# Kernel optimization log

Measured on AMD Instinct MI355X. Metric: run time of the kernel, lower is better.

The kernel has to match this reference:

```python
import jax, jax.numpy as jnp
import numpy as np

BEAM = 3
MAX_LENGTH = 32
START = 1


def setup_inputs() -> dict:
    key = jax.random.key(0)
    ks = jax.random.split(key, 10)
    B, S, H, E, V = 32, 64, 512, 256, 32000
    sE = 1.0 / np.sqrt(E)
    sH = 1.0 / np.sqrt(H)
    return {
        "encoder_outputs": jax.random.normal(ks[0], (B, S, H), jnp.float32),
        "encoder_hidden": jax.random.normal(ks[1], (B, H), jnp.float32),
        "emb": jax.random.normal(ks[2], (V, E), jnp.float32) * 0.02,
        "W_ih": jax.random.uniform(ks[3], (3 * H, E), jnp.float32, -sE, sE),
        "W_hh": jax.random.uniform(ks[4], (3 * H, H), jnp.float32, -sH, sH),
        "b_ih": jax.random.uniform(ks[5], (3 * H,), jnp.float32, -sH, sH),
        "b_hh": jax.random.uniform(ks[6], (3 * H,), jnp.float32, -sH, sH),
        "W_out": jax.random.uniform(ks[7], (V, H), jnp.float32, -sH, sH),
        "b_out": jax.random.uniform(ks[8], (V,), jnp.float32, -sH, sH),
    }


def _gru_cell(x, h, W_ih, W_hh, b_ih, b_hh):
    # PyTorch GRU cell math. x: (N,E), h: (N,H)
    gi = x @ W_ih.T + b_ih          # (N, 3H)
    gh = h @ W_hh.T + b_hh          # (N, 3H)
    i_r, i_z, i_n = jnp.split(gi, 3, axis=-1)
    h_r, h_z, h_n = jnp.split(gh, 3, axis=-1)
    r = jax.nn.sigmoid(i_r + h_r)
    z = jax.nn.sigmoid(i_z + h_z)
    n = jnp.tanh(i_n + r * h_n)
    return (1.0 - z) * n + z * h


def reference(encoder_outputs, encoder_hidden, emb, W_ih, W_hh, b_ih, b_hh, W_out, b_out):
    B = encoder_outputs.shape[0]
    K = BEAM
    V, H = W_out.shape
    BK = B * K

    # expand encoder hidden for beams: each batch row repeated K times
    h0 = jnp.repeat(encoder_hidden, K, axis=0)                 # (BK, H)
    tok0 = jnp.full((BK,), START, jnp.int32)
    seqs0 = jnp.full((BK, MAX_LENGTH + 1), START, jnp.int32)   # col 0 = start token
    scores0 = jnp.zeros((BK,), jnp.float32)
    brow = jnp.arange(B)[:, None] * K                          # (B,1)

    def step(carry, t):
        tok, h, seqs, scores = carry
        x = jax.nn.relu(emb[tok])                              # (BK, E) gather + relu
        h_new = _gru_cell(x, h, W_ih, W_hh, b_ih, b_hh)        # (BK, H)
        logits = h_new @ W_out.T + b_out                       # (BK, V)
        logp = jax.nn.log_softmax(logits, axis=-1)
        next_scores, next_tokens = jax.lax.top_k(logp, K)      # (BK, K)
        total = scores.reshape(B, K, 1) + next_scores.reshape(B, K, K)
        top_scores, top_idx = jax.lax.top_k(total.reshape(B, K * K), K)  # (B, K)
        beam_idx = top_idx // K
        tok_idx = top_idx % K
        old = (brow + beam_idx).reshape(-1)                    # (BK,) source beam rows
        new_tok = next_tokens[old, tok_idx.reshape(-1)].astype(jnp.int32)
        h2 = h_new[old]
        seqs2 = jax.lax.dynamic_update_slice(seqs[old], new_tok[:, None], (0, t + 1))
        return (new_tok, h2, seqs2, top_scores.reshape(-1)), None

    (tok, h, seqs, scores), _ = jax.lax.scan(
        step, (tok0, h0, seqs0, scores0), jnp.arange(MAX_LENGTH))

    # beam 0 is best (top_k is sorted descending)
    best_seqs = seqs.reshape(B, K, MAX_LENGTH + 1)[:, 0]       # (B, L+1)
    decoded = jax.nn.one_hot(best_seqs, V, dtype=jnp.float32)  # (B, L+1, V)
    return decoded, h.reshape(B, K, H), scores.reshape(B, K)
```

## Files before the change

kernel.cpp:

```cpp
#include <hip/hip_runtime.h>
#include <float.h>
#include <math.h>


#define BB 32
#define HH 512
#define EE 256
#define VV 32000
#define TSTEPS 32
#define NCH 500
#define PSTR 512
#define DEC_ELEMS (BB * (TSTEPS + 1) * VV)
#define H_ELEMS (BB * 3 * HH)
#define SMEM_FLOATS 18432
#define HB (BB * HH)
#define SB (BB * PSTR)

__device__ __forceinline__ void st_agent(float* p, float v) {
  __hip_atomic_store(p, v, __ATOMIC_RELAXED, __HIP_MEMORY_SCOPE_AGENT);
}
__device__ __forceinline__ void st_agent_i(int* p, int v) {
  __hip_atomic_store(p, v, __ATOMIC_RELAXED, __HIP_MEMORY_SCOPE_AGENT);
}

__global__ __launch_bounds__(256) void k_transpose_out(
    const float* __restrict__ W, float* __restrict__ Wt) {
  __shared__ float t[32][33];
  const int vb = blockIdx.x * 32;
  const int kb = blockIdx.y * 32;
  const int c = threadIdx.x & 31, rq = threadIdx.x >> 5;
#pragma unroll
  for (int i = 0; i < 4; ++i) {
    int r = rq + i * 8;
    t[r][c] = W[(size_t)(vb + r) * HH + kb + c];
  }
  __syncthreads();
#pragma unroll
  for (int i = 0; i < 4; ++i) {
    int r = rq + i * 8;
    Wt[(size_t)(kb + r) * VV + vb + c] = t[c][r];
  }
}

__global__ __launch_bounds__(256) void k_init(
    const float* __restrict__ enc_h, float* __restrict__ h0,
    float* __restrict__ scores, int* __restrict__ tok_seq,
    unsigned* __restrict__ bar) {
  int idx = blockIdx.x * 256 + threadIdx.x;
  if (idx < BB * HH) h0[idx] = enc_h[idx];
  if (idx < BB) { scores[idx] = 0.0f; tok_seq[idx] = 1; }
  if (idx == 0) { bar[0] = 0u; bar[32] = 0u; }
}

__device__ __forceinline__ void gbar(unsigned* bar, unsigned nblk) {
  __syncthreads();
  if (threadIdx.x == 0) {
    asm volatile("s_waitcnt vmcnt(0)" ::: "memory");
    unsigned g = __hip_atomic_load(&bar[32], __ATOMIC_RELAXED,
                                   __HIP_MEMORY_SCOPE_AGENT);
    asm volatile("s_waitcnt vmcnt(0)" ::: "memory");
    unsigned a = __hip_atomic_fetch_add(&bar[0], 1u, __ATOMIC_RELAXED,
                                        __HIP_MEMORY_SCOPE_AGENT);
    if (a == nblk - 1u) {
      __hip_atomic_store(&bar[0], 0u, __ATOMIC_RELAXED,
                         __HIP_MEMORY_SCOPE_AGENT);
      asm volatile("s_waitcnt vmcnt(0)" ::: "memory");
      __hip_atomic_fetch_add(&bar[32], 1u, __ATOMIC_RELAXED,
                             __HIP_MEMORY_SCOPE_AGENT);
    } else {
      while (__hip_atomic_load(&bar[32], __ATOMIC_RELAXED,
                               __HIP_MEMORY_SCOPE_AGENT) == g)
        __builtin_amdgcn_s_sleep(2);
    }
  }
  __syncthreads();
}

#define FMA4(accv, hscal, wv)              \
  accv.x = fmaf(hscal, wv.x, accv.x);      \
  accv.y = fmaf(hscal, wv.y, accv.y);      \
  accv.z = fmaf(hscal, wv.z, accv.z);      \
  accv.w = fmaf(hscal, wv.w, accv.w);

#define LOADG(W, g)                                                    \
  {                                                                    \
    const float* p_ = wp + (size_t)(g) * 8 * VV;                       \
    _Pragma("unroll") for (int j_ = 0; j_ < 8; ++j_)                   \
        W[j_] = *(const float4*)(p_ + (size_t)j_ * VV);                \
  }

#define COMPG(W, g)                                                    \
  {                                                                    \
    const int k0_ = (g) * 8;                                           \
    _Pragma("unroll") for (int jj_ = 0; jj_ < 2; ++jj_) {              \
      const float4 h0_ = *(const float4*)&hs[r0][k0_ + jj_ * 4];       \
      const float4 h1_ = *(const float4*)&hs[r0 + 1][k0_ + jj_ * 4];   \
      FMA4(acc0, h0_.x, W[jj_ * 4 + 0]);                               \
      FMA4(acc0, h0_.y, W[jj_ * 4 + 1]);                               \
      FMA4(acc0, h0_.z, W[jj_ * 4 + 2]);                               \
      FMA4(acc0, h0_.w, W[jj_ * 4 + 3]);                               \
      FMA4(acc1, h1_.x, W[jj_ * 4 + 0]);                               \
      FMA4(acc1, h1_.y, W[jj_ * 4 + 1]);                               \
      FMA4(acc1, h1_.z, W[jj_ * 4 + 2]);                               \
      FMA4(acc1, h1_.w, W[jj_ * 4 + 3]);                               \
    }                                                                  \
  }

__device__ __forceinline__ void gemv_body_glb(
    const int vb, const int tid, float* smem,
    const float* __restrict__ Wt, const float* __restrict__ hmat,
    const float* __restrict__ bout,
    float* __restrict__ pm, float* __restrict__ ps, int* __restrict__ pidx) {
  const int colq = tid & 15;
  const int rp = tid >> 4;
  const int r0 = rp * 2;
  const int col = vb * 64 + colq * 4;

  float (*hs)[516] = (float(*)[516])smem;
  {
    float4* hd = (float4*)smem;
    const float4* hp = (const float4*)hmat;
#pragma unroll
    for (int i = 0; i < 16; ++i) {
      const int idx = i * 256 + tid;
      const int r = idx >> 7, q = idx & 127;
      hd[r * 129 + q] = hp[idx];
    }
  }
  __syncthreads();

  const float* wp = Wt + col;
  float4 acc0 = {0.0f, 0.0f, 0.0f, 0.0f};
  float4 acc1 = {0.0f, 0.0f, 0.0f, 0.0f};

  float4 A[8], B[8], C[8];
  LOADG(A, 0);
  LOADG(B, 1);
#pragma unroll 1
  for (int g = 0; g < 63; g += 3) {
    LOADG(C, g + 2);
    COMPG(A, g);
    if (g + 3 < 64) LOADG(A, g + 3);
    COMPG(B, g + 1);
    if (g + 4 < 64) LOADG(B, g + 4);
    COMPG(C, g + 2);
  }
  COMPG(A, 63);

  {
    const float4 bo = *(const float4*)(bout + col);
    acc0.x += bo.x; acc0.y += bo.y; acc0.z += bo.z; acc0.w += bo.w;
    acc1.x += bo.x; acc1.y += bo.y; acc1.z += bo.z; acc1.w += bo.w;
  }

  const int lane = tid & 63;
  float m0 = acc0.x; int i0 = col;
  if (acc0.y > m0) { m0 = acc0.y; i0 = col + 1; }
  if (acc0.z > m0) { m0 = acc0.z; i0 = col + 2; }
  if (acc0.w > m0) { m0 = acc0.w; i0 = col + 3; }
  float m1 = acc1.x; int i1 = col;
  if (acc1.y > m1) { m1 = acc1.y; i1 = col + 1; }
  if (acc1.z > m1) { m1 = acc1.z; i1 = col + 2; }
  if (acc1.w > m1) { m1 = acc1.w; i1 = col + 3; }
#pragma unroll
  for (int off = 1; off < 16; off <<= 1) {
    const float om0 = __shfl_xor(m0, off);
    const int oi0 = __shfl_xor(i0, off);
    if (om0 > m0 || (om0 == m0 && oi0 < i0)) { m0 = om0; i0 = oi0; }
    const float om1 = __shfl_xor(m1, off);
    const int oi1 = __shfl_xor(i1, off);
    if (om1 > m1 || (om1 == m1 && oi1 < i1)) { m1 = om1; i1 = oi1; }
  }
  float s0 = __expf(acc0.x - m0) + __expf(acc0.y - m0) +
             __expf(acc0.z - m0) + __expf(acc0.w - m0);
  float s1 = __expf(acc1.x - m1) + __expf(acc1.y - m1) +
             __expf(acc1.z - m1) + __expf(acc1.w - m1);
#pragma unroll
  for (int off = 1; off < 16; off <<= 1) {
    s0 += __shfl_xor(s0, off);
    s1 += __shfl_xor(s1, off);
  }
  if ((lane & 15) == 0) {
    st_agent(&pm[r0 * PSTR + vb], m0);
    st_agent(&ps[r0 * PSTR + vb], s0);
    st_agent_i(&pidx[r0 * PSTR + vb], i0);
    st_agent(&pm[(r0 + 1) * PSTR + vb], m1);
    st_agent(&ps[(r0 + 1) * PSTR + vb], s1);
    st_agent_i(&pidx[(r0 + 1) * PSTR + vb], i1);
  }
}

__device__ __forceinline__ void gru_body(
    const int bid, const int tid, const int step, float* smem, int* toks,
    const float* __restrict__ emb,
    const float* __restrict__ W_ih,
    const float* __restrict__ W_hh,
    const float* __restrict__ b_ih, const float* __restrict__ b_hh,
    const float* __restrict__ hin, float* __restrict__ hout,
    const float* __restrict__ pmt, const float* __restrict__ pst,
    const int* __restrict__ pidxt,
    float* __restrict__ scores, int* __restrict__ tok_seq) {
  const int rg = bid >> 4;
  const int jt = bid & 15;
  const int r0 = rg * 4, j0 = jt * 32;
  const int lane = tid & 63, wv = tid >> 6;

  float (*xs)[EE] = (float(*)[EE])smem;
  float (*hsm)[HH] = (float(*)[HH])(smem + 4 * EE);
  float* gpart = smem + 4 * EE + 4 * HH;

  if (step == 0) {
    if (tid < 4) toks[tid] = 1;
  } else {
    const int row = r0 + wv;
    float mv[8], sv[8];
    int iv[8];
#pragma unroll
    for (int j = 0; j < 8; ++j) {
      const int ch = lane + 64 * j;
      const bool v = (ch < NCH);
      mv[j] = v ? pmt[row * PSTR + ch] : -FLT_MAX;
      sv[j] = v ? pst[row * PSTR + ch] : 0.0f;
      iv[j] = v ? pidxt[row * PSTR + ch] : 0x7fffffff;
    }
    float gm = mv[0];
    int gi = iv[0];
#pragma unroll
    for (int j = 1; j < 8; ++j)
      if (mv[j] > gm || (mv[j] == gm && iv[j] < gi)) { gm = mv[j]; gi = iv[j]; }
#pragma unroll
    for (int off = 1; off < 64; off <<= 1) {
      const float om = __shfl_xor(gm, off);
      const int oi = __shfl_xor(gi, off);
      if (om > gm || (om == gm && oi < gi)) { gm = om; gi = oi; }
    }
    float term = 0.0f;
#pragma unroll
    for (int j = 0; j < 8; ++j) term += sv[j] * __expf(mv[j] - gm);
#pragma unroll
    for (int off = 1; off < 64; off <<= 1) term += __shfl_xor(term, off);
    if (lane == 0) {
      toks[wv] = gi;
      if (jt == 0) {
        scores[row] -= logf(term);
        tok_seq[step * BB + row] = gi;
      }
    }
  }
  __syncthreads();
  if (step == TSTEPS) return;

  for (int i = tid; i < 4 * EE; i += 256) {
    const int r = i >> 8, c = i & (EE - 1);
    const float e = emb[(size_t)toks[r] * EE + c];
    xs[r][c] = e > 0.0f ? e : 0.0f;
  }
  for (int i = tid; i < 4 * HH; i += 256) {
    const int r = i >> 9, c = i & (HH - 1);
    hsm[r][c] = hin[(r0 + r) * HH + c];
  }
  __syncthreads();

  const int jh = tid & 31, kq = tid >> 5;
  const int j = j0 + jh;
  float ai[3][4], ah[3][4];
#pragma unroll
  for (int g = 0; g < 3; ++g)
#pragma unroll
    for (int r = 0; r < 4; ++r) { ai[g][r] = 0.0f; ah[g][r] = 0.0f; }

#pragma unroll 2
  for (int q = 0; q < 8; ++q) {
    const int k4 = kq * 32 + q * 4;
    float4 xr[4];
#pragma unroll
    for (int r = 0; r < 4; ++r) xr[r] = *(const float4*)&xs[r][k4];
#pragma unroll
    for (int g = 0; g < 3; ++g) {
      const float4 w = *(const float4*)&W_ih[(size_t)(g * HH + j) * EE + k4];
#pragma unroll
      for (int r = 0; r < 4; ++r) {
        ai[g][r] = fmaf(xr[r].x, w.x, ai[g][r]);
        ai[g][r] = fmaf(xr[r].y, w.y, ai[g][r]);
        ai[g][r] = fmaf(xr[r].z, w.z, ai[g][r]);
        ai[g][r] = fmaf(xr[r].w, w.w, ai[g][r]);
      }
    }
  }
#pragma unroll 2
  for (int q = 0; q < 16; ++q) {
    const int k4 = kq * 64 + q * 4;
    float4 hr[4];
#pragma unroll
    for (int r = 0; r < 4; ++r) hr[r] = *(const float4*)&hsm[r][k4];
#pragma unroll
    for (int g = 0; g < 3; ++g) {
      const float4 w = *(const float4*)&W_hh[(size_t)(g * HH + j) * HH + k4];
#pragma unroll
      for (int r = 0; r < 4; ++r) {
        ah[g][r] = fmaf(hr[r].x, w.x, ah[g][r]);
        ah[g][r] = fmaf(hr[r].y, w.y, ah[g][r]);
        ah[g][r] = fmaf(hr[r].z, w.z, ah[g][r]);
        ah[g][r] = fmaf(hr[r].w, w.w, ah[g][r]);
      }
    }
  }
  {
    const int base = kq * 34 + jh;
#pragma unroll
    for (int g = 0; g < 3; ++g)
#pragma unroll
      for (int r = 0; r < 4; ++r) {
        gpart[(g * 4 + r) * 272 + base] = ai[g][r];
        gpart[(12 + g * 4 + r) * 272 + base] = ah[g][r];
      }
  }
  __syncthreads();

  if (tid < 128) {
    const int r = tid >> 5, jh2 = tid & 31;
    const int j2 = j0 + jh2;
    float g6[6];
#pragma unroll
    for (int c = 0; c < 6; ++c) {
      const int cc = (c < 3) ? (c * 4 + r) : (12 + (c - 3) * 4 + r);
      float s = 0.0f;
#pragma unroll
      for (int q = 0; q < 8; ++q) s += gpart[cc * 272 + q * 34 + jh2];
      g6[c] = s;
    }
    const float ir = g6[0] + b_ih[j2];
    const float iz = g6[1] + b_ih[HH + j2];
    const float in_ = g6[2] + b_ih[2 * HH + j2];
    const float hr_ = g6[3] + b_hh[j2];
    const float hz = g6[4] + b_hh[HH + j2];
    const float hn = g6[5] + b_hh[2 * HH + j2];
    const float rr = 1.0f / (1.0f + expf(-(ir + hr_)));
    const float zz = 1.0f / (1.0f + expf(-(iz + hz)));
    const float nn = tanhf(in_ + rr * hn);
    st_agent(&hout[(r0 + r) * HH + j2], (1.0f - zz) * nn + zz * hsm[r][j2]);
  }
}

__global__ __launch_bounds__(256, 2) void k_persist(
    const float* __restrict__ Wt, const float* __restrict__ emb,
    const float* __restrict__ W_ih, const float* __restrict__ W_hh,
    const float* __restrict__ b_ih, const float* __restrict__ b_hh,
    const float* __restrict__ bout,
    float* hseq, float* pmT, float* psT, int* pidxT,
    float* scores, int* tok_seq, unsigned* bar) {
  __shared__ __align__(16) float smem[SMEM_FLOATS];
  __shared__ int toks[4];
  const int bid = blockIdx.x, tid = threadIdx.x;
  const int c2 = tid & 31, kq = tid >> 5;
  const int vb = bid;

  float2 wreg[64];
  if (vb < NCH) {
    const float* wp = Wt + (size_t)(kq * 64) * VV + vb * 64 + c2 * 2;
#pragma unroll
    for (int k = 0; k < 64; ++k)
      wreg[k] = *(const float2*)(wp + (size_t)k * VV);
  } else {
#pragma unroll
    for (int k = 0; k < 64; ++k) wreg[k] = make_float2(0.0f, 0.0f);
  }
  float2 bo = make_float2(0.0f, 0.0f);
  if (vb < NCH) bo = *(const float2*)(bout + vb * 64 + c2 * 2);

  float* hs = smem;
  float* part = smem + 16384;

  for (int t = 0; t <= TSTEPS; ++t) {
    const float* hin = hseq + (size_t)t * HB;
    float* hout = hseq + (size_t)(t + 1) * HB;
    const int tp = (t > 0) ? (t - 1) : 0;
    if (bid < 128)
      gru_body(bid, tid, t, smem, toks, emb, W_ih, W_hh, b_ih, b_hh,
               hin, hout, pmT + (size_t)tp * SB, psT + (size_t)tp * SB,
               pidxT + (size_t)tp * SB, scores, tok_seq);
    gbar(bar, 512u);
    if (t == TSTEPS) break;

    if (vb < NCH) {
      float* pm = pmT + (size_t)t * SB;
      float* ps = psT + (size_t)t * SB;
      int* pidx = pidxT + (size_t)t * SB;
      {
        float4* hd = (float4*)hs;
        const float4* hp = (const float4*)hout;
#pragma unroll
        for (int i = 0; i < 16; ++i) hd[i * 256 + tid] = hp[i * 256 + tid];
      }
      __syncthreads();

      const int w = tid >> 6;
      const int rr = tid >> 5;
      const int cp = tid & 31;
#pragma unroll 1
      for (int rc = 0; rc < 4; ++rc) {
        float acc0[8], acc1[8];
#pragma unroll
        for (int r = 0; r < 8; ++r) { acc0[r] = 0.0f; acc1[r] = 0.0f; }
#pragma unroll
        for (int r = 0; r < 8; ++r) {
          const float* hrow = hs + (rc * 8 + r) * 512 + kq * 64;
#pragma unroll
          for (int j = 0; j < 16; ++j) {
            const float4 h4 = *(const float4*)(hrow + j * 4);
            acc0[r] = fmaf(h4.x, wreg[j * 4 + 0].x, acc0[r]);
            acc1[r] = fmaf(h4.x, wreg[j * 4 + 0].y, acc1[r]);
            acc0[r] = fmaf(h4.y, wreg[j * 4 + 1].x, acc0[r]);
            acc1[r] = fmaf(h4.y, wreg[j * 4 + 1].y, acc1[r]);
            acc0[r] = fmaf(h4.z, wreg[j * 4 + 2].x, acc0[r]);
            acc1[r] = fmaf(h4.z, wreg[j * 4 + 2].y, acc1[r]);
            acc0[r] = fmaf(h4.w, wreg[j * 4 + 3].x, acc0[r]);
            acc1[r] = fmaf(h4.w, wreg[j * 4 + 3].y, acc1[r]);
          }
        }
#pragma unroll
        for (int r = 0; r < 8; ++r) {
          acc0[r] += __shfl_xor(acc0[r], 32);
          acc1[r] += __shfl_xor(acc1[r], 32);
        }
        if ((tid & 32) == 0) {
#pragma unroll
          for (int r = 0; r < 8; ++r) {
            float2* pp = (float2*)&part[w * 512 + r * 64 + c2 * 2];
            *pp = make_float2(acc0[r], acc1[r]);
          }
        }
        __syncthreads();
        {
          float l0 = 0.0f, l1 = 0.0f;
#pragma unroll
          for (int ww = 0; ww < 4; ++ww) {
            const float2 p = *(const float2*)&part[ww * 512 + rr * 64 + cp * 2];
            l0 += p.x; l1 += p.y;
          }
          const float2 bb = *(const float2*)(bout + vb * 64 + cp * 2);
          l0 += bb.x; l1 += bb.y;
          const int col0 = vb * 64 + cp * 2;
          float m = l0; int ii = col0;
          if (l1 > m) { m = l1; ii = col0 + 1; }
#pragma unroll
          for (int off = 1; off < 32; off <<= 1) {
            const float om = __shfl_xor(m, off);
            const int oi = __shfl_xor(ii, off);
            if (om > m || (om == m && oi < ii)) { m = om; ii = oi; }
          }
          float e = __expf(l0 - m) + __expf(l1 - m);
#pragma unroll
          for (int off = 1; off < 32; off <<= 1) e += __shfl_xor(e, off);
          if (cp == 0) {
            const int grow = rc * 8 + rr;
            st_agent(&pm[grow * PSTR + vb], m);
            st_agent(&ps[grow * PSTR + vb], e);
            st_agent_i(&pidx[grow * PSTR + vb], ii);
          }
        }
        __syncthreads();
      }
    }
    gbar(bar, 512u);
  }
  (void)bo;
}

__global__ __launch_bounds__(256) void k_gemv_fused(
    const float* __restrict__ Wt, const float* __restrict__ hmat,
    const float* __restrict__ bout,
    float* __restrict__ pm, float* __restrict__ ps, int* __restrict__ pidx) {
  __shared__ __align__(16) float smem[16512];
  gemv_body_glb(blockIdx.x, threadIdx.x, smem, Wt, hmat, bout, pm, ps, pidx);
}

__global__ __launch_bounds__(256) void k_gru(
    const int step, const float* __restrict__ emb,
    const float* __restrict__ W_ih, const float* __restrict__ W_hh,
    const float* __restrict__ b_ih, const float* __restrict__ b_hh,
    const float* __restrict__ hin, float* __restrict__ hout,
    const float* __restrict__ pmt, const float* __restrict__ pst,
    const int* __restrict__ pidxt,
    float* __restrict__ scores, int* __restrict__ tok_seq) {
  __shared__ __align__(16) float smem[9600];
  __shared__ int toks[4];
  gru_body(blockIdx.x, threadIdx.x, step, smem, toks, emb, W_ih, W_hh,
           b_ih, b_hh, hin, hout, pmt, pst, pidxt, scores, tok_seq);
}

__global__ __launch_bounds__(256) void k_out(
    const int* __restrict__ tok_seq, const float* __restrict__ hfin,
    const float* __restrict__ scores, float* __restrict__ out) {
  const int blk = blockIdx.x, tid = threadIdx.x;
  if (blk < BB * (TSTEPS + 1)) {
    const int b = blk / (TSTEPS + 1), t = blk % (TSTEPS + 1);
    const int tok = tok_seq[t * BB + b];
    const int tq = tok >> 2, tl = tok & 3;
    float4* op = (float4*)(out + (size_t)blk * VV);
    for (int i = tid; i < VV / 4; i += 256) {
      float4 z = {0.0f, 0.0f, 0.0f, 0.0f};
      if (i == tq) (&z.x)[tl] = 1.0f;
      op[i] = z;
    }
  } else if (blk < BB * (TSTEPS + 1) + 12) {
#pragma unroll
    for (int it = 0; it < 4; ++it) {
      const int idx = (blk - BB * (TSTEPS + 1)) * 1024 + it * 256 + tid;
      if (idx < H_ELEMS / 4) {
        const int fi = idx * 4;
        const int b = fi / (3 * HH);
        const int j0 = (fi % (3 * HH)) % HH;
        ((float4*)(out + DEC_ELEMS))[idx] =
            *(const float4*)(hfin + b * HH + j0);
      }
    }
  } else {
    if (tid < BB * 3) {
      out[(size_t)DEC_ELEMS + H_ELEMS + tid] = scores[tid / 3];
    }
  }
}

extern "C" void kernel_launch(void* const* d_in, const int* in_sizes, int n_in,
                              void* d_out, int out_size, void* d_ws, size_t ws_size,
                              hipStream_t stream) {
  const float* enc_h = (const float*)d_in[1];
  const float* emb   = (const float*)d_in[2];
  const float* W_ih  = (const float*)d_in[3];
  const float* W_hh  = (const float*)d_in[4];
  const float* b_ih  = (const float*)d_in[5];
  const float* b_hh  = (const float*)d_in[6];
  const float* W_out = (const float*)d_in[7];
  const float* b_out = (const float*)d_in[8];
  float* out = (float*)d_out;

  float* ws = (float*)d_ws;
  float* Wt_out  = ws;
  float* hseq    = Wt_out + 16384000;
  float* pmT     = hseq + 34 * HB;
  float* psT     = pmT + 32 * SB;
  float* scores  = psT + 32 * SB;
  int*   pidxT   = (int*)(scores + BB);
  int*   tok_seq = pidxT + 32 * SB;
  unsigned* bar  = (unsigned*)(tok_seq + BB * (TSTEPS + 1));

  k_transpose_out<<<dim3(1000, 16), 256, 0, stream>>>(W_out, Wt_out);
  k_init<<<64, 256, 0, stream>>>(enc_h, hseq, scores, tok_seq, bar);

  const float* Wt_c = Wt_out;
  void* args[] = {(void*)&Wt_c,  (void*)&emb,  (void*)&W_ih, (void*)&W_hh,
                  (void*)&b_ih,  (void*)&b_hh, (void*)&b_out,
                  (void*)&hseq,  (void*)&pmT,  (void*)&psT,  (void*)&pidxT,
                  (void*)&scores, (void*)&tok_seq, (void*)&bar};
  hipError_t ce = hipLaunchCooperativeKernel(
      reinterpret_cast<const void*>(&k_persist), dim3(512), dim3(256),
      args, 0u, stream);

  if (ce != hipSuccess) {
    for (int t = 0; t < TSTEPS; ++t) {
      const int tp = (t > 0) ? (t - 1) : 0;
      k_gru<<<128, 256, 0, stream>>>(
          t, emb, W_ih, W_hh, b_ih, b_hh,
          hseq + (size_t)t * HB, hseq + (size_t)(t + 1) * HB,
          pmT + (size_t)tp * SB, psT + (size_t)tp * SB,
          pidxT + (size_t)tp * SB, scores, tok_seq);
      k_gemv_fused<<<NCH, 256, 0, stream>>>(
          Wt_out, hseq + (size_t)(t + 1) * HB, b_out,
          pmT + (size_t)t * SB, psT + (size_t)t * SB,
          pidxT + (size_t)t * SB);
    }
    k_gru<<<128, 256, 0, stream>>>(
        TSTEPS, emb, W_ih, W_hh, b_ih, b_hh,
        hseq + (size_t)TSTEPS * HB, hseq + (size_t)(TSTEPS + 1) * HB,
        pmT + (size_t)(TSTEPS - 1) * SB, psT + (size_t)(TSTEPS - 1) * SB,
        pidxT + (size_t)(TSTEPS - 1) * SB, scores, tok_seq);
  }

  k_out<<<BB * (TSTEPS + 1) + 13, 256, 0, stream>>>(
      tok_seq, hseq + (size_t)TSTEPS * HB, scores, out);
}
```

Before: 1.779 ms.

## Replace global grid barriers with per-step producer/consumer flag slots

The two all-block grid barriers per step become single-use counters in per-timestep slots. GRU blocks (0-127) arrive in groups of 16 and vocab blocks arrive in groups of 64. A last-arriver tree then sets eight separate ready flags, and consumers poll the flag for their group. Only producers and consumers of each stage now take part, idle blocks do not join the barrier, and there is no shared generation counter. The cost is a larger sync region that must be zeroed at init, and correctness depends on the group counts matching the block partition.

```diff
diff --git a/kernel.cpp b/kernel.cpp
--- a/kernel.cpp
+++ b/kernel.cpp
@@ -15,12 +15,43 @@
 #define SMEM_FLOATS 18432
 #define HB (BB * HH)
 #define SB (BB * PSTR)
+#define SLOT_U 1024
+#define NSLOT 64
 
 __device__ __forceinline__ void st_agent(float* p, float v) {
   __hip_atomic_store(p, v, __ATOMIC_RELAXED, __HIP_MEMORY_SCOPE_AGENT);
 }
 __device__ __forceinline__ void st_agent_i(int* p, int v) {
   __hip_atomic_store(p, v, __ATOMIC_RELAXED, __HIP_MEMORY_SCOPE_AGENT);
+}
+
+__device__ __forceinline__ void sync_arrive(unsigned* slot, int g,
+                                            unsigned gtgt) {
+  __syncthreads();
+  if (threadIdx.x == 0) {
+    asm volatile("s_waitcnt vmcnt(0)" ::: "memory");
+    unsigned a = __hip_atomic_fetch_add(&slot[g * 32], 1u, __ATOMIC_RELAXED,
+                                        __HIP_MEMORY_SCOPE_AGENT);
+    if (a == gtgt - 1u) {
+      unsigned r = __hip_atomic_fetch_add(&slot[256], 1u, __ATOMIC_RELAXED,
+                                          __HIP_MEMORY_SCOPE_AGENT);
+      if (r == 7u) {
+#pragma unroll
+        for (int i = 0; i < 8; ++i)
+          __hip_atomic_store(&slot[512 + i * 32], 1u, __ATOMIC_RELAXED,
+                             __HIP_MEMORY_SCOPE_AGENT);
+      }
+    }
+  }
+}
+
+__device__ __forceinline__ void sync_wait(unsigned* slot, int g) {
+  if (threadIdx.x == 0) {
+    while (__hip_atomic_load(&slot[512 + g * 32], __ATOMIC_RELAXED,
+                             __HIP_MEMORY_SCOPE_AGENT) == 0u)
+      __builtin_amdgcn_s_sleep(4);
+  }
+  __syncthreads();
 }
 
 __global__ __launch_bounds__(256) void k_transpose_out(
@@ -45,35 +76,11 @@
 __global__ __launch_bounds__(256) void k_init(
     const float* __restrict__ enc_h, float* __restrict__ h0,
     float* __restrict__ scores, int* __restrict__ tok_seq,
-    unsigned* __restrict__ bar) {
+    unsigned* __restrict__ sync) {
   int idx = blockIdx.x * 256 + threadIdx.x;
   if (idx < BB * HH) h0[idx] = enc_h[idx];
   if (idx < BB) { scores[idx] = 0.0f; tok_seq[idx] = 1; }
-  if (idx == 0) { bar[0] = 0u; bar[32] = 0u; }
-}
-
-__device__ __forceinline__ void gbar(unsigned* bar, unsigned nblk) {
-  __syncthreads();
-  if (threadIdx.x == 0) {
-    asm volatile("s_waitcnt vmcnt(0)" ::: "memory");
-    unsigned g = __hip_atomic_load(&bar[32], __ATOMIC_RELAXED,
-                                   __HIP_MEMORY_SCOPE_AGENT);
-    asm volatile("s_waitcnt vmcnt(0)" ::: "memory");
-    unsigned a = __hip_atomic_fetch_add(&bar[0], 1u, __ATOMIC_RELAXED,
-                                        __HIP_MEMORY_SCOPE_AGENT);
-    if (a == nblk - 1u) {
-      __hip_atomic_store(&bar[0], 0u, __ATOMIC_RELAXED,
-                         __HIP_MEMORY_SCOPE_AGENT);
-      asm volatile("s_waitcnt vmcnt(0)" ::: "memory");
-      __hip_atomic_fetch_add(&bar[32], 1u, __ATOMIC_RELAXED,
-                             __HIP_MEMORY_SCOPE_AGENT);
-    } else {
-      while (__hip_atomic_load(&bar[32], __ATOMIC_RELAXED,
-                               __HIP_MEMORY_SCOPE_AGENT) == g)
-        __builtin_amdgcn_s_sleep(2);
-    }
-  }
-  __syncthreads();
+  for (int i = idx; i < NSLOT * SLOT_U; i += 16384) sync[i] = 0u;
 }
 
 #define FMA4(accv, hscal, wv)              \
@@ -348,7 +355,7 @@
     const float* __restrict__ b_ih, const float* __restrict__ b_hh,
     const float* __restrict__ bout,
     float* hseq, float* pmT, float* psT, int* pidxT,
-    float* scores, int* tok_seq, unsigned* bar) {
+    float* scores, int* tok_seq, unsigned* sync) {
   __shared__ __align__(16) float smem[SMEM_FLOATS];
   __shared__ int toks[4];
   const int bid = blockIdx.x, tid = threadIdx.x;
@@ -365,8 +372,6 @@
 #pragma unroll
     for (int k = 0; k < 64; ++k) wreg[k] = make_float2(0.0f, 0.0f);
   }
-  float2 bo = make_float2(0.0f, 0.0f);
-  if (vb < NCH) bo = *(const float2*)(bout + vb * 64 + c2 * 2);
 
   float* hs = smem;
   float* part = smem + 16384;
@@ -375,14 +380,19 @@
     const float* hin = hseq + (size_t)t * HB;
     float* hout = hseq + (size_t)(t + 1) * HB;
     const int tp = (t > 0) ? (t - 1) : 0;
-    if (bid < 128)
+
+    if (bid < 128) {
+      if (t > 0) sync_wait(sync + (size_t)(32 + tp) * SLOT_U, bid & 7);
       gru_body(bid, tid, t, smem, toks, emb, W_ih, W_hh, b_ih, b_hh,
                hin, hout, pmT + (size_t)tp * SB, psT + (size_t)tp * SB,
                pidxT + (size_t)tp * SB, scores, tok_seq);
-    gbar(bar, 512u);
+      if (t < TSTEPS)
+        sync_arrive(sync + (size_t)t * SLOT_U, bid >> 4, 16u);
+    }
     if (t == TSTEPS) break;
 
     if (vb < NCH) {
+      sync_wait(sync + (size_t)t * SLOT_U, bid & 7);
       float* pm = pmT + (size_t)t * SB;
       float* ps = psT + (size_t)t * SB;
       int* pidx = pidxT + (size_t)t * SB;
@@ -461,10 +471,10 @@
         }
         __syncthreads();
       }
-    }
-    gbar(bar, 512u);
-  }
-  (void)bo;
+      sync_arrive(sync + (size_t)(32 + t) * SLOT_U, bid >> 6,
+                  (bid >> 6) < 7 ? 64u : 52u);
+    }
+  }
 }
 
 __global__ __launch_bounds__(256) void k_gemv_fused(
@@ -543,16 +553,16 @@
   float* scores  = psT + 32 * SB;
   int*   pidxT   = (int*)(scores + BB);
   int*   tok_seq = pidxT + 32 * SB;
-  unsigned* bar  = (unsigned*)(tok_seq + BB * (TSTEPS + 1));
+  unsigned* sync = (unsigned*)(tok_seq + BB * (TSTEPS + 1));
 
   k_transpose_out<<<dim3(1000, 16), 256, 0, stream>>>(W_out, Wt_out);
-  k_init<<<64, 256, 0, stream>>>(enc_h, hseq, scores, tok_seq, bar);
+  k_init<<<64, 256, 0, stream>>>(enc_h, hseq, scores, tok_seq, sync);
 
   const float* Wt_c = Wt_out;
   void* args[] = {(void*)&Wt_c,  (void*)&emb,  (void*)&W_ih, (void*)&W_hh,
                   (void*)&b_ih,  (void*)&b_hh, (void*)&b_out,
                   (void*)&hseq,  (void*)&pmT,  (void*)&psT,  (void*)&pidxT,
-                  (void*)&scores, (void*)&tok_seq, (void*)&bar};
+                  (void*)&scores, (void*)&tok_seq, (void*)&sync};
   hipError_t ce = hipLaunchCooperativeKernel(
       reinterpret_cast<const void*>(&k_persist), dim3(512), dim3(256),
       args, 0u, stream);
```

New measurement: 1.605 ms. 1.11x faster.
